# Kernel optimization log

Measured on AMD Instinct MI355X. Metric: run time of the kernel, lower is better.

## Reference

```python
import jax, jax.numpy as jnp
import numpy as np
from jax import lax

EPS = 1e-20  # matches sample_gumbel eps in the TF source


def setup_inputs() -> dict:
    key = jax.random.key(0)
    ks = jax.random.split(key, 7)
    B, T, D, H, K = 32, 512, 512, 512, 64
    x = jax.random.normal(ks[0], (B, T, D), jnp.float32)
    f_after = jax.random.normal(ks[1], (K, D, H), jnp.float32) * 0.02
    f_skip = jax.random.normal(ks[2], (2 * H, 2), jnp.float32) * 0.05
    gru_kernel = jax.random.normal(ks[3], (D, 3 * H), jnp.float32) * 0.02
    gru_rec_kernel = jax.random.normal(ks[4], (H, 3 * H), jnp.float32) * 0.02
    gru_bias = jnp.zeros((2, 3 * H), jnp.float32)
    u_gumbel = jax.random.uniform(ks[5], (T, B, 2), jnp.float32)
    return {"x": x, "f_after": f_after, "f_skip": f_skip,
            "gru_kernel": gru_kernel, "gru_rec_kernel": gru_rec_kernel,
            "gru_bias": gru_bias, "u_gumbel": u_gumbel}


def reference(x, f_after, f_skip, gru_kernel, gru_rec_kernel, gru_bias, u_gumbel):
    # z_after = tanh(conv1d(x, f_after, SAME))  -> [B, T, H]
    z_after = lax.conv_general_dilated(
        x, f_after, window_strides=(1,), padding='SAME',
        dimension_numbers=('NWC', 'WIO', 'NWC'))
    z_after = jnp.tanh(z_after)

    # gumbel(0,1) noise from uniform draws, per step: [T, B, 2]
    g = -jnp.log(-jnp.log(u_gumbel + EPS) + EPS)

    b_in, b_rec = gru_bias[0], gru_bias[1]  # reset_after=True biases, each [3H]
    H = gru_rec_kernel.shape[0]
    B = x.shape[0]
    h0 = jnp.zeros((B, H), x.dtype)

    xs = (jnp.swapaxes(x, 0, 1), jnp.swapaxes(z_after, 0, 1), g)  # time-major

    def step(h_prev, inp):
        x_t, za_t, g_t = inp
        # skip gate: concat(h_{t-1}, z_after_t) @ f_skip, gumbel-softmax (temp=1)
        logits = jnp.concatenate([h_prev, za_t], axis=-1) @ f_skip  # [B, 2]
        skip = jax.nn.softmax(logits + g_t, axis=-1)
        # Keras GRUCell (reset_after=True), gate order z, r, h
        xm = x_t @ gru_kernel + b_in          # [B, 3H]
        hm = h_prev @ gru_rec_kernel + b_rec  # [B, 3H]
        xz, xr, xh = jnp.split(xm, 3, axis=-1)
        hz, hr, hh = jnp.split(hm, 3, axis=-1)
        z = jax.nn.sigmoid(xz + hz)
        r = jax.nn.sigmoid(xr + hr)
        hc = jnp.tanh(xh + r * hh)
        ht = z * h_prev + (1.0 - z) * hc
        # skip blend
        ht = skip[:, 0:1] * h_prev + skip[:, 1:2] * ht
        return ht, ht

    _, ys = lax.scan(step, h0, xs)           # [T, B, H]
    return jnp.swapaxes(ys, 0, 1)            # [B, T, H]
```

## Files before the change

### kernel.cpp

```cpp
#include <hip/hip_runtime.h>
#include <stdint.h>

typedef unsigned short u16;
typedef unsigned int   u32;
typedef __attribute__((ext_vector_type(8))) short short8;
typedef __attribute__((ext_vector_type(4))) float f32x4;
typedef __attribute__((ext_vector_type(4))) u32   u32x4;

#define AS1 __attribute__((address_space(1)))
#define AS3 __attribute__((address_space(3)))

#define SENT 0x7FC0u

__device__ __forceinline__ float bf2f(u16 u) {
  union { u32 i; float f; } v; v.i = ((u32)u) << 16; return v.f;
}
__device__ __forceinline__ u16 f2bf(float f) {
  union { float f; u32 i; } v; v.f = f;
  u32 i = v.i;
  i += 0x7FFFu + ((i >> 16) & 1u);
  return (u16)(i >> 16);
}
__device__ __forceinline__ float tanh_fast(float x) {
  const float e = __expf(-2.f * fabsf(x));
  const float t = (1.f - e) / (1.f + e);
  return __builtin_copysignf(t, x);
}

__device__ __forceinline__ void gload16(const u16* src, u16* ldsDst) {
  __builtin_amdgcn_global_load_lds((const AS1 u32*)src, (AS3 u32*)ldsDst, 16, 0, 0);
}

__device__ __forceinline__ short8 ldg_sc_h_wait(const u16* p) {
  short8 r;
  asm volatile("global_load_dwordx4 %0, %1, off sc0 sc1\n\t"
               "s_waitcnt vmcnt(0)"
               : "=v"(r) : "v"(p) : "memory");
  return r;
}
__device__ __forceinline__ void stg_sc_h(u16* p, u16 v) {
  asm volatile("global_store_short %0, %1, off sc0 sc1" :: "v"(p), "v"((u32)v) : "memory");
}

__global__ void k_init(const float* __restrict__ x, u16* __restrict__ xp) {
  const long NXP = 32L * 576 * 512;
  long i0 = (long)blockIdx.x * 256 + threadIdx.x;
  for (long i = i0; i < NXP; i += (long)gridDim.x * 256) {
    long b = i / (576 * 512);
    int rem = (int)(i - b * (576 * 512));
    int rr = rem >> 9, dd = rem & 511;
    int t = rr - 31;
    float v = (t >= 0 && t < 512) ? x[(b * 512 + t) * 512 + dd] : 0.f;
    xp[i] = f2bf(v);
  }
}

__global__ void k_sent(u32* __restrict__ hs) {
  const u32x4 s = u32x4{(SENT << 16) | SENT, (SENT << 16) | SENT,
                        (SENT << 16) | SENT, (SENT << 16) | SENT};
  *(u32x4*)&hs[((long)blockIdx.x * 256 + threadIdx.x) * 4] = s;
}

__global__ void k_transpose_cast(const float* __restrict__ in, u16* __restrict__ out,
                                 int rows, int cols, long inWStride, long outWStride) {
  __shared__ float tile[64][65];
  const int w = blockIdx.z;
  const float* ip = in + (long)w * inWStride;
  u16* op = out + (long)w * outWStride;
  const int r0 = blockIdx.y * 64, c0 = blockIdx.x * 64;
  const int tr = threadIdx.x >> 6, tc = threadIdx.x & 63;
  #pragma unroll
  for (int p = 0; p < 16; ++p) {
    int rr = p * 4 + tr;
    tile[rr][tc] = ip[(long)(r0 + rr) * cols + c0 + tc];
  }
  __syncthreads();
  #pragma unroll
  for (int p = 0; p < 16; ++p) {
    int rr = p * 4 + tr;
    op[(long)(c0 + rr) * rows + r0 + tc] = f2bf(tile[tc][rr]);
  }
}

__global__ __launch_bounds__(256) void k_gemm(
    const u16* __restrict__ A, const u16* __restrict__ Bm, u16* __restrict__ C,
    int nTiles, int kw, int woff, long bWStride, int outMode)
{
  __shared__ __align__(16) u16 Alds[128 * 64];
  __shared__ __align__(16) u16 Blds[128 * 64];
  const int bid = blockIdx.x;
  const int mt = bid / nTiles, nt = bid - mt * nTiles;
  const int bb = (mt * 128) >> 9;
  const int t0 = (mt * 128) & 511;
  const int h0 = nt * 128;
  const int tid = threadIdx.x;
  const int wv = tid >> 6, l = tid & 63;
  const int wr = wv >> 1, wc = wv & 1;
  const int sRow = wv * 8 + (l >> 3);
  const int sCol = (l & 7) * 8;
  f32x4 acc[4][4];
  #pragma unroll
  for (int m = 0; m < 4; ++m)
    #pragma unroll
    for (int n = 0; n < 4; ++n) acc[m][n] = f32x4{0.f, 0.f, 0.f, 0.f};

  const int kIters = kw * 8;
  const long aRow0 = (long)(bb * 576 + t0 + woff);
  for (int q = 0; q < kIters; ++q) {
    const int w = q >> 3, dsub = (q & 7) << 6;
    const u16* aB = A + (aRow0 + w) * 512 + dsub + sCol;
    const u16* bB = Bm + (long)w * bWStride + (long)h0 * 512 + dsub + sCol;
    __syncthreads();
    #pragma unroll
    for (int c = 0; c < 4; ++c) {
      gload16(aB + (long)(c * 32 + sRow) * 512, &Alds[c * 2048 + wv * 512]);
      gload16(bB + (long)(c * 32 + sRow) * 512, &Blds[c * 2048 + wv * 512]);
    }
    __syncthreads();
    #pragma unroll
    for (int kk = 0; kk < 2; ++kk) {
      short8 af[4], bf[4];
      #pragma unroll
      for (int m = 0; m < 4; ++m)
        af[m] = *(const short8*)&Alds[(wr * 64 + m * 16 + (l & 15)) * 64 + kk * 32 + (l >> 4) * 8];
      #pragma unroll
      for (int n = 0; n < 4; ++n)
        bf[n] = *(const short8*)&Blds[(wc * 64 + n * 16 + (l & 15)) * 64 + kk * 32 + (l >> 4) * 8];
      #pragma unroll
      for (int m = 0; m < 4; ++m)
        #pragma unroll
        for (int n = 0; n < 4; ++n)
          acc[m][n] = __builtin_amdgcn_mfma_f32_16x16x32_bf16(af[m], bf[n], acc[m][n], 0, 0, 0);
    }
  }
  const int lr = (l >> 4) * 4, lc = l & 15;
  #pragma unroll
  for (int m = 0; m < 4; ++m)
    #pragma unroll
    for (int n = 0; n < 4; ++n)
      #pragma unroll
      for (int r = 0; r < 4; ++r) {
        const int row = mt * 128 + wr * 64 + m * 16 + lr + r;
        const int col = h0 + wc * 64 + n * 16 + lc;
        const float v = acc[m][n][r];
        if (outMode == 0) {
          C[(long)row * 512 + col] = f2bf(tanhf(v));
        } else {
          const int b = row >> 9, t = row & 511;
          C[((long)t * 32 + b) * 1536 + col] = f2bf(v);
        }
      }
}

__global__ void k_dza(const u16* __restrict__ za, const float* __restrict__ fskip,
                      const float* __restrict__ ug, float* __restrict__ dza) {
  __shared__ float wd2[512];
  const int t = blockIdx.x, tid = threadIdx.x;
  for (int i = tid; i < 512; i += 256) wd2[i] = fskip[(512 + i) * 2 + 1] - fskip[(512 + i) * 2];
  __syncthreads();
  const int b = tid >> 3, seg = (tid & 7) * 64;
  const u16* row = za + ((long)b * 512 + t) * 512 + seg;
  float pp = 0.f;
  #pragma unroll
  for (int j = 0; j < 8; ++j) {
    short8 v = *(const short8*)&row[j * 8];
    #pragma unroll
    for (int e = 0; e < 8; ++e) pp += bf2f((u16)v[e]) * wd2[seg + j * 8 + e];
  }
  pp += __shfl_xor(pp, 1); pp += __shfl_xor(pp, 2); pp += __shfl_xor(pp, 4);
  if ((tid & 7) == 0) {
    float u0 = ug[((long)t * 32 + b) * 2 + 0], u1 = ug[((long)t * 32 + b) * 2 + 1];
    float g0 = -logf(-logf(u0 + 1e-20f) + 1e-20f);
    float g1 = -logf(-logf(u1 + 1e-20f) + 1e-20f);
    dza[t * 32 + b] = pp + (g1 - g0);
  }
}

__global__ __launch_bounds__(256, 1) void k_rnn(
    const u16* __restrict__ XM, const float* __restrict__ dza,
    const float* __restrict__ Wrec, const float* __restrict__ gbias,
    const float* __restrict__ fskip, u16* hstep, float* __restrict__ out)
{
  const int bid = blockIdx.x, d = bid & 7, s = bid >> 3;
  const int tid = threadIdx.x, wv = tid >> 6, l = tid & 63;
  __shared__ __align__(16) u16 hBl[2][2048];

  const int colb = s * 64 + wv * 16 + (l & 15);
  const int kq = (l >> 4) * 8;

  short8 wf[3][16];
  #pragma unroll
  for (int g = 0; g < 3; ++g)
    #pragma unroll
    for (int kk = 0; kk < 16; ++kk) {
      short8 tmp;
      #pragma unroll
      for (int e = 0; e < 8; ++e)
        tmp[e] = (short)f2bf(Wrec[(long)(kk * 32 + kq + e) * 1536 + g * 512 + colb]);
      wf[g][kk] = tmp;
    }
  short8 wdf[16];
  #pragma unroll
  for (int kk = 0; kk < 16; ++kk) {
    short8 tmp;
    #pragma unroll
    for (int e = 0; e < 8; ++e) {
      const int k = kk * 32 + kq + e;
      tmp[e] = (short)f2bf(fskip[k * 2 + 1] - fskip[k * 2]);
    }
    wdf[kk] = tmp;
  }
  float bi[3], br[3];
  #pragma unroll
  for (int g = 0; g < 3; ++g) {
    bi[g] = gbias[g * 512 + colb];
    br[g] = gbias[1536 + g * 512 + colb];
  }
  const int myb = d * 4;
  float hp[4] = {0.f, 0.f, 0.f, 0.f};

  u16 xmc[3][4]; f32x4 dzc;
  if (l < 16) {
    const u16* xr = XM + (long)myb * 1536;
    #pragma unroll
    for (int r = 0; r < 4; ++r)
      #pragma unroll
      for (int g = 0; g < 3; ++g)
        xmc[g][r] = xr[(long)r * 1536 + g * 512 + colb];
    dzc = *(const f32x4*)&dza[myb];
  }

  for (int t = 0; t < 512; ++t) {
    const int p = t & 1;

    short8 h8;
    if (t > 0) {
      const u16* ph = hstep + ((long)(t - 1) * 32 + myb + wv) * 512 + l * 8;
      h8 = ldg_sc_h_wait(ph);
      bool bad = true;
      while (bad) {
        bad = false;
        #pragma unroll
        for (int e = 0; e < 8; ++e) bad |= ((u16)h8[e] == SENT);
        if (bad) h8 = ldg_sc_h_wait(ph);
      }
    } else {
      #pragma unroll
      for (int e = 0; e < 8; ++e) h8[e] = 0;
    }

    u16 xmn[3][4]; f32x4 dzn;
    const int tn = (t < 511) ? t + 1 : t;
    if (l < 16) {
      const u16* xr = XM + ((long)tn * 32 + myb) * 1536;
      #pragma unroll
      for (int r = 0; r < 4; ++r)
        #pragma unroll
        for (int g = 0; g < 3; ++g)
          xmn[g][r] = xr[(long)r * 1536 + g * 512 + colb];
      dzn = *(const f32x4*)&dza[tn * 32 + myb];
    }

    *(short8*)&hBl[p][tid * 8] = h8;
    __syncthreads();

    f32x4 acc[4];
    acc[0] = f32x4{0.f, 0.f, 0.f, 0.f};
    acc[1] = acc[0]; acc[2] = acc[0]; acc[3] = acc[0];
    const int b4 = l & 3;
    #pragma unroll
    for (int kk = 0; kk < 16; ++kk) {
      short8 a = *(const short8*)&hBl[p][b4 * 512 + kk * 32 + kq];
      acc[0] = __builtin_amdgcn_mfma_f32_16x16x32_bf16(a, wf[0][kk], acc[0], 0, 0, 0);
      acc[1] = __builtin_amdgcn_mfma_f32_16x16x32_bf16(a, wf[1][kk], acc[1], 0, 0, 0);
      acc[2] = __builtin_amdgcn_mfma_f32_16x16x32_bf16(a, wf[2][kk], acc[2], 0, 0, 0);
      acc[3] = __builtin_amdgcn_mfma_f32_16x16x32_bf16(a, wdf[kk],  acc[3], 0, 0, 0);
    }

    if (l < 16) {
      #pragma unroll
      for (int r = 0; r < 4; ++r) {
        const float xz = bf2f(xmc[0][r]) + bi[0];
        const float xr_ = bf2f(xmc[1][r]) + bi[1];
        const float xh = bf2f(xmc[2][r]) + bi[2];
        const float hz = acc[0][r] + br[0];
        const float hr = acc[1][r] + br[1];
        const float hh = acc[2][r] + br[2];
        const float z  = 1.f / (1.f + __expf(-(xz + hz)));
        const float rr = 1.f / (1.f + __expf(-(xr_ + hr)));
        const float hc = tanh_fast(xh + rr * hh);
        const float ht = z * hp[r] + (1.f - z) * hc;
        const float s1 = 1.f / (1.f + __expf(-(acc[3][r] + dzc[r])));
        const float hn = hp[r] + s1 * (ht - hp[r]);
        stg_sc_h(&hstep[((long)t * 32 + myb + r) * 512 + colb], f2bf(hn));
        hp[r] = hn;
      }
      #pragma unroll
      for (int r = 0; r < 4; ++r)
        out[((long)(myb + r) * 512 + t) * 512 + colb] = hp[r];
      #pragma unroll
      for (int g = 0; g < 3; ++g)
        #pragma unroll
        for (int r = 0; r < 4; ++r) xmc[g][r] = xmn[g][r];
      dzc = dzn;
    }
  }
}

extern "C" void kernel_launch(void* const* d_in, const int* in_sizes, int n_in,
                              void* d_out, int out_size, void* d_ws, size_t ws_size,
                              hipStream_t stream) {
  (void)in_sizes; (void)n_in; (void)out_size; (void)ws_size;
  const float* x        = (const float*)d_in[0];
  const float* f_after  = (const float*)d_in[1];
  const float* f_skip   = (const float*)d_in[2];
  const float* gru_k    = (const float*)d_in[3];
  const float* gru_rec  = (const float*)d_in[4];
  const float* gru_bias = (const float*)d_in[5];
  const float* ug       = (const float*)d_in[6];
  float* out = (float*)d_out;

  char* ws = (char*)d_ws;
  size_t off = 0;
  auto alloc = [&](size_t bytes) { void* p = ws + off; off = (off + bytes + 255) & ~(size_t)255; return p; };
  u16*  xp    = (u16*)alloc(32L * 576 * 512 * 2);
  u16*  fT    = (u16*)alloc(64L * 512 * 512 * 2);
  u16*  gruT  = (u16*)alloc(1536L * 512 * 2);
  u16*  za    = (u16*)alloc(32L * 512 * 512 * 2);
  u16*  XM    = (u16*)alloc(512L * 32 * 1536 * 2);
  float* dza  = (float*)alloc(512L * 32 * 4);
  u16*  hstep = za;

  k_init<<<dim3(4096), dim3(256), 0, stream>>>(x, xp);
  k_transpose_cast<<<dim3(8, 8, 64), dim3(256), 0, stream>>>(f_after, fT, 512, 512, 512L * 512, 512L * 512);
  k_transpose_cast<<<dim3(24, 8, 1), dim3(256), 0, stream>>>(gru_k, gruT, 512, 1536, 0L, 0L);
  k_gemm<<<dim3(512), dim3(256), 0, stream>>>(xp, fT, za, 4, 64, 0, 512L * 512, 0);
  k_gemm<<<dim3(1536), dim3(256), 0, stream>>>(xp, gruT, XM, 12, 1, 31, 0L, 1);
  k_dza<<<dim3(512), dim3(256), 0, stream>>>(za, f_skip, ug, dza);
  k_sent<<<dim3(4096), dim3(256), 0, stream>>>((u32*)hstep);
  k_rnn<<<dim3(64), dim3(256), 0, stream>>>(XM, dza, gru_rec, gru_bias, f_skip, hstep, out);
}
```

Measured before the change: 2.333 ms.

## Compute skip gate via wave reduction, pad LDS rows, defer output stores, swizzle GEMM blocks

The recurrent kernel drops the fourth MFMA chain and the wdf register array for the skip-gate dot product. Each wave instead reduces its own batch row with a shuffle reduction and shares the sigmoid result through shared memory. The h tile in LDS gets padded rows to avoid bank conflicts, and the output store for step t is delayed to the next iteration so it leaves the critical path after the hstep publish. The GEMM kernel also remaps block ids across 8 groups, likely to spread tiles across XCDs for cache locality.

```diff
diff --git a/kernel.cpp b/kernel.cpp
--- a/kernel.cpp
+++ b/kernel.cpp
@@ -11,6 +11,7 @@
 #define AS3 __attribute__((address_space(3)))
 
 #define SENT 0x7FC0u
+#define HS   528
 
 __device__ __forceinline__ float bf2f(u16 u) {
   union { u32 i; float f; } v; v.i = ((u32)u) << 16; return v.f;
@@ -88,7 +89,9 @@
 {
   __shared__ __align__(16) u16 Alds[128 * 64];
   __shared__ __align__(16) u16 Blds[128 * 64];
-  const int bid = blockIdx.x;
+  const int bid0 = blockIdx.x;
+  const int cpx = gridDim.x >> 3;
+  const int bid = (bid0 & 7) * cpx + (bid0 >> 3);
   const int mt = bid / nTiles, nt = bid - mt * nTiles;
   const int bb = (mt * 128) >> 9;
   const int t0 = (mt * 128) & 511;
@@ -183,7 +186,13 @@
 {
   const int bid = blockIdx.x, d = bid & 7, s = bid >> 3;
   const int tid = threadIdx.x, wv = tid >> 6, l = tid & 63;
-  __shared__ __align__(16) u16 hBl[2][2048];
+  __shared__ __align__(16) u16 hBl[2][4 * HS];
+  __shared__ float s1s[2][4];
+
+  float wdv[8];
+  #pragma unroll
+  for (int e = 0; e < 8; ++e)
+    wdv[e] = fskip[(l * 8 + e) * 2 + 1] - fskip[(l * 8 + e) * 2];
 
   const int colb = s * 64 + wv * 16 + (l & 15);
   const int kq = (l >> 4) * 8;
@@ -199,17 +208,6 @@
         tmp[e] = (short)f2bf(Wrec[(long)(kk * 32 + kq + e) * 1536 + g * 512 + colb]);
       wf[g][kk] = tmp;
     }
-  short8 wdf[16];
-  #pragma unroll
-  for (int kk = 0; kk < 16; ++kk) {
-    short8 tmp;
-    #pragma unroll
-    for (int e = 0; e < 8; ++e) {
-      const int k = kk * 32 + kq + e;
-      tmp[e] = (short)f2bf(fskip[k * 2 + 1] - fskip[k * 2]);
-    }
-    wdf[kk] = tmp;
-  }
   float bi[3], br[3];
   #pragma unroll
   for (int g = 0; g < 3; ++g) {
@@ -218,8 +216,10 @@
   }
   const int myb = d * 4;
   float hp[4] = {0.f, 0.f, 0.f, 0.f};
-
-  u16 xmc[3][4]; f32x4 dzc;
+  float hnv[4] = {0.f, 0.f, 0.f, 0.f};
+
+  u16 xmc[3][4];
+  float dzc;
   if (l < 16) {
     const u16* xr = XM + (long)myb * 1536;
     #pragma unroll
@@ -227,8 +227,8 @@
       #pragma unroll
       for (int g = 0; g < 3; ++g)
         xmc[g][r] = xr[(long)r * 1536 + g * 512 + colb];
-    dzc = *(const f32x4*)&dza[myb];
-  }
+  }
+  dzc = dza[myb + wv];
 
   for (int t = 0; t < 512; ++t) {
     const int p = t & 1;
@@ -249,7 +249,13 @@
       for (int e = 0; e < 8; ++e) h8[e] = 0;
     }
 
-    u16 xmn[3][4]; f32x4 dzn;
+    if (t > 0 && l < 16) {
+      #pragma unroll
+      for (int r = 0; r < 4; ++r)
+        out[((long)(myb + r) * 512 + (t - 1)) * 512 + colb] = hnv[r];
+    }
+
+    u16 xmn[3][4];
     const int tn = (t < 511) ? t + 1 : t;
     if (l < 16) {
       const u16* xr = XM + ((long)tn * 32 + myb) * 1536;
@@ -258,23 +264,27 @@
         #pragma unroll
         for (int g = 0; g < 3; ++g)
           xmn[g][r] = xr[(long)r * 1536 + g * 512 + colb];
-      dzn = *(const f32x4*)&dza[tn * 32 + myb];
-    }
-
-    *(short8*)&hBl[p][tid * 8] = h8;
+    }
+    const float dzn = dza[tn * 32 + myb + wv];
+
+    *(short8*)&hBl[p][wv * HS + l * 8] = h8;
+    float pp = 0.f;
+    #pragma unroll
+    for (int e = 0; e < 8; ++e) pp += bf2f((u16)h8[e]) * wdv[e];
+    #pragma unroll
+    for (int o = 1; o < 64; o <<= 1) pp += __shfl_xor(pp, o);
+    if (l == 0) s1s[p][wv] = 1.f / (1.f + __expf(-(pp + dzc)));
     __syncthreads();
 
-    f32x4 acc[4];
-    acc[0] = f32x4{0.f, 0.f, 0.f, 0.f};
-    acc[1] = acc[0]; acc[2] = acc[0]; acc[3] = acc[0];
+    f32x4 acc[3];
+    acc[0] = f32x4{0.f, 0.f, 0.f, 0.f}; acc[1] = acc[0]; acc[2] = acc[0];
     const int b4 = l & 3;
     #pragma unroll
     for (int kk = 0; kk < 16; ++kk) {
-      short8 a = *(const short8*)&hBl[p][b4 * 512 + kk * 32 + kq];
+      short8 a = *(const short8*)&hBl[p][b4 * HS + kk * 32 + kq];
       acc[0] = __builtin_amdgcn_mfma_f32_16x16x32_bf16(a, wf[0][kk], acc[0], 0, 0, 0);
       acc[1] = __builtin_amdgcn_mfma_f32_16x16x32_bf16(a, wf[1][kk], acc[1], 0, 0, 0);
       acc[2] = __builtin_amdgcn_mfma_f32_16x16x32_bf16(a, wf[2][kk], acc[2], 0, 0, 0);
-      acc[3] = __builtin_amdgcn_mfma_f32_16x16x32_bf16(a, wdf[kk],  acc[3], 0, 0, 0);
     }
 
     if (l < 16) {
@@ -290,20 +300,23 @@
         const float rr = 1.f / (1.f + __expf(-(xr_ + hr)));
         const float hc = tanh_fast(xh + rr * hh);
         const float ht = z * hp[r] + (1.f - z) * hc;
-        const float s1 = 1.f / (1.f + __expf(-(acc[3][r] + dzc[r])));
+        const float s1 = s1s[p][r];
         const float hn = hp[r] + s1 * (ht - hp[r]);
         stg_sc_h(&hstep[((long)t * 32 + myb + r) * 512 + colb], f2bf(hn));
         hp[r] = hn;
+        hnv[r] = hn;
       }
-      #pragma unroll
-      for (int r = 0; r < 4; ++r)
-        out[((long)(myb + r) * 512 + t) * 512 + colb] = hp[r];
       #pragma unroll
       for (int g = 0; g < 3; ++g)
         #pragma unroll
         for (int r = 0; r < 4; ++r) xmc[g][r] = xmn[g][r];
-      dzc = dzn;
-    }
+    }
+    dzc = dzn;
+  }
+  if (l < 16) {
+    #pragma unroll
+    for (int r = 0; r < 4; ++r)
+      out[((long)(myb + r) * 512 + 511) * 512 + colb] = hnv[r];
   }
 }
 
```

Measured after the change: 2.111 ms. -9.5%, faster.
